# Kernel optimization log

Hardware: AMD Instinct MI355X
Metric: run time of the kernel (lower is better)

The kernel has to match this reference:

```python
import jax, jax.numpy as jnp
import numpy as np
from jax import lax

KSIZE, STRIDE, RATE, FUSE_K, SCALE, FUSE = 3, 1, 2, 3, 10.0, True


def _same_pad(h, w, k, s):
    oh, ow = -(-h // s), -(-w // s)
    ph = max(0, (oh - 1) * s + k - h)
    pw = max(0, (ow - 1) * s + k - w)
    return (ph // 2, ph - ph // 2), (pw // 2, pw - pw // 2), oh, ow


def extract_patches(x, k, s):
    # x: [B,C,H,W] -> ([B, L, C, k, k], Ho, Wo); matches torch Unfold with 'same' padding
    B, C, H, W = x.shape
    (pt, pb), (pl, pr), Ho, Wo = _same_pad(H, W, k, s)
    xp = jnp.pad(x, ((0, 0), (0, 0), (pt, pb), (pl, pr)))
    rows = []
    for i in range(k):
        cols = [xp[:, :, i:i + s * (Ho - 1) + 1:s, j:j + s * (Wo - 1) + 1:s] for j in range(k)]
        rows.append(jnp.stack(cols, axis=2))  # [B,C,k,Ho,Wo]
    pat = jnp.stack(rows, axis=2)  # [B,C,k,k,Ho,Wo]
    pat = pat.reshape(B, C, k, k, Ho * Wo).transpose(0, 4, 1, 2, 3)
    return pat, Ho, Wo


def setup_inputs() -> dict:
    key = jax.random.key(0)
    kf, kb = jax.random.split(key)
    f = jax.random.normal(kf, (2, 128, 64, 64), dtype=jnp.float32)
    b = jax.random.normal(kb, (2, 128, 64, 64), dtype=jnp.float32)
    mask = jnp.zeros((2, 1, 256, 256), dtype=jnp.float32)
    return {"f": f, "b": b, "mask": mask}


def _forward(f, b, mask):
    B, C, Hr, Wr = f.shape
    kernel = 2 * RATE
    # raw background patches used as deconv kernels: [B, L, C, 4, 4]
    raw_w, _, _ = extract_patches(b, kernel, RATE * STRIDE)
    # nearest 1/rate downsample (torch nearest picks every rate-th pixel)
    fd = f[:, :, ::RATE, ::RATE]
    bd = b[:, :, ::RATE, ::RATE]
    Hf, Wf = fd.shape[2], fd.shape[3]
    Hb, Wb = bd.shape[2], bd.shape[3]
    L = Hb * Wb
    w, _, _ = extract_patches(bd, KSIZE, STRIDE)  # [B, L, C, 3, 3]
    # mask -> validity per background patch (original uses batch 0's mask only)
    md = mask[:, :, ::4 * RATE, ::4 * RATE]
    m, _, _ = extract_patches(md, KSIZE, STRIDE)  # [B, L, 1, 3, 3]
    mm = (jnp.mean(m[0], axis=(1, 2, 3)) == 0.0).astype(f.dtype)  # [L]
    # l2-normalize patch kernels (escape_NaN added per element before sum, as in torch)
    wn = w / jnp.sqrt(jnp.sum(w * w + 1e-4, axis=(2, 3, 4), keepdims=True))
    # correlation conv == batched GEMM over extracted foreground patches
    fp, _, _ = extract_patches(fd, KSIZE, 1)  # [B, P=Hf*Wf, C, 3, 3]
    scores = jnp.einsum('bpckl,bqckl->bqp', fp, wn)  # [B, L, Hf*Wf]
    scores = scores.reshape(B, Hb, Wb, Hf, Wf)

    if FUSE:
        def fuse_diag(y2):  # conv with 3x3 identity kernel, same pad == 3 diagonal shifts
            yp = jnp.pad(y2, ((1, 1), (1, 1)))
            return yp[:-2, :-2] + yp[1:-1, 1:-1] + yp[2:, 2:]

        def fuse_one(s):  # [Hb,Wb,Hf,Wf]
            y = fuse_diag(s.reshape(Hb * Wb, Hf * Wf)).reshape(Hb, Wb, Hf, Wf)
            y = y.transpose(1, 0, 3, 2)
            y = fuse_diag(y.reshape(Wb * Hb, Wf * Hf)).reshape(Wb, Hb, Wf, Hf)
            return y.transpose(1, 0, 3, 2)

        scores = jax.vmap(fuse_one)(scores)

    yi = scores.reshape(B, L, Hf, Wf) * mm[None, :, None, None]
    yi = jax.nn.softmax(yi * SCALE, axis=1) * mm[None, :, None, None]

    # transposed conv with per-batch raw patches as kernels (stride=rate, padding=1), /4
    def deconv_one(attn, wpat):  # attn [L,Hf,Wf], wpat [L,C,4,4]
        rhs = jnp.flip(wpat, axis=(2, 3)).transpose(1, 0, 2, 3)  # [C, L, 4, 4]
        pad = kernel - 1 - 1  # equivalent VALID padding for transposed conv with padding=1
        out = lax.conv_general_dilated(attn[None], rhs, (1, 1),
                                       padding=((pad, pad), (pad, pad)),
                                       lhs_dilation=(RATE, RATE),
                                       dimension_numbers=('NCHW', 'OIHW', 'NCHW'))
        return out[0] / 4.0

    y = jax.vmap(deconv_one)(yi, raw_w)  # [B, C, Hr, Wr]
    return y


def reference(f, b, mask):
    return _forward(f, b, mask)
```

## Files before the change

### kernel.cpp

```cpp
#include <hip/hip_runtime.h>
#include <hip/hip_bf16.h>
#include <math.h>

constexpr int HS = 32;
constexpr int Lq = 1024;
constexpr int CN = 128;

typedef short bf16x8 __attribute__((ext_vector_type(8)));
typedef float f32x4  __attribute__((ext_vector_type(4)));

__device__ inline unsigned short f2bf(float x) {
    union { float f; unsigned int u; } c; c.f = x;
    return (unsigned short)((c.u + 0x7FFF + ((c.u >> 16) & 1)) >> 16);
}
__device__ inline float bf2f(unsigned short h) {
    union { unsigned int u; float f; } c; c.u = ((unsigned int)h) << 16;
    return c.f;
}

__global__ __launch_bounds__(256) void k_prep3(const float* __restrict__ f,
                                               const float* __restrict__ bsrc,
                                               unsigned short* __restrict__ fH, unsigned short* __restrict__ fL,
                                               unsigned short* __restrict__ bH, unsigned short* __restrict__ bL,
                                               float* __restrict__ ssq,
                                               unsigned short* __restrict__ Wm) {
    int tx = threadIdx.x;
    if (blockIdx.x < 512) {
        int u = blockIdx.x * 4 + (tx >> 6);
        int lane = tx & 63;
        int p = u & (Lq - 1), bb = u >> 10;
        int py = p >> 5, px = p & 31;
        long srcbase = (((long)bb * CN) * 64 + 2 * py) * 64 + 2 * px;
        float s = 0.f;
#pragma unroll
        for (int i = 0; i < 2; ++i) {
            int c = lane + i * 64;
            long src = srcbase + (long)c * 4096;
            float fv = f[src], bv = bsrc[src];
            int o = u * CN + c;
            unsigned short fh = f2bf(fv), bh = f2bf(bv);
            fH[o] = fh; fL[o] = f2bf(fv - bf2f(fh));
            bH[o] = bh; bL[o] = f2bf(bv - bf2f(bh));
            s += bv * bv;
        }
        for (int off = 32; off > 0; off >>= 1) s += __shfl_down(s, off, 64);
        if (lane == 0) ssq[u] = s;
    } else {
        int idx = (blockIdx.x - 512) * 256 + tx;
        int q  = idx & (Lq - 1);
        int m  = (idx >> 10) & 2047;
        int bb = idx >> 21;
        int c = m >> 4, u = (m >> 2) & 3, v = m & 3;
        int qy = q >> 5, qx = q & 31;
        int y = 2 * qy + u - 1, x = 2 * qx + v - 1;
        float val = 0.f;
        if ((unsigned)y < 64u && (unsigned)x < 64u)
            val = bsrc[(((long)bb * CN + c) * 64 + y) * 64 + x];
        Wm[idx] = f2bf(val);
    }
}

__global__ __launch_bounds__(256) void k_nm(const float* __restrict__ ssq, const float* __restrict__ mask,
                                            float* __restrict__ norms, float* __restrict__ mmb) {
    int idx = blockIdx.x * 256 + threadIdx.x;
    if (idx < 2048) {
        int q = idx & (Lq - 1);
        int bb = idx >> 10;
        int qy = q >> 5, qx = q & 31;
        float s = 0.1152f;
        for (int dk = -1; dk <= 1; ++dk) {
            int y = qy + dk; if ((unsigned)y >= (unsigned)HS) continue;
            for (int dl = -1; dl <= 1; ++dl) {
                int x = qx + dl; if ((unsigned)x >= (unsigned)HS) continue;
                s += ssq[bb * Lq + y * HS + x];
            }
        }
        norms[idx] = sqrtf(s);
    } else {
        int q = idx - 2048;
        int qy = q >> 5, qx = q & 31;
        float s = 0.f;
        for (int dk = -1; dk <= 1; ++dk) {
            int y = qy + dk; if ((unsigned)y >= (unsigned)HS) continue;
            for (int dl = -1; dl <= 1; ++dl) {
                int x = qx + dl; if ((unsigned)x >= (unsigned)HS) continue;
                s += mask[(8 * y) * 256 + 8 * x];
            }
        }
        mmb[q] = (s == 0.0f) ? 1.0f : 0.0f;
    }
}

__global__ __launch_bounds__(256) void k_gram(const unsigned short* __restrict__ fH,
                                              const unsigned short* __restrict__ fL,
                                              const unsigned short* __restrict__ bH,
                                              const unsigned short* __restrict__ bL,
                                              float* __restrict__ GT) {
    const long bz = blockIdx.z;
    const unsigned short* AH = fH + bz * 131072;
    const unsigned short* AL = fL + bz * 131072;
    const unsigned short* BH = bH + bz * 131072;
    const unsigned short* BL = bL + bz * 131072;
    float* C = GT + (bz << 20);
    int t = threadIdx.x, w = t >> 6, lane = t & 63, quad = lane >> 4, l16 = lane & 15;
    int wm = blockIdx.x * 64 + (w & 1) * 32;
    int wn = blockIdx.y * 64 + (w >> 1) * 32;
    int ko = quad * 8;
    f32x4 acc[2][2] = {};
#pragma unroll
    for (int k0 = 0; k0 < 128; k0 += 32) {
        bf16x8 ah0 = *(const bf16x8*)&AH[(wm + l16) * 128 + ko + k0];
        bf16x8 ah1 = *(const bf16x8*)&AH[(wm + 16 + l16) * 128 + ko + k0];
        bf16x8 al0 = *(const bf16x8*)&AL[(wm + l16) * 128 + ko + k0];
        bf16x8 al1 = *(const bf16x8*)&AL[(wm + 16 + l16) * 128 + ko + k0];
        bf16x8 bh0 = *(const bf16x8*)&BH[(wn + l16) * 128 + ko + k0];
        bf16x8 bh1 = *(const bf16x8*)&BH[(wn + 16 + l16) * 128 + ko + k0];
        bf16x8 bl0 = *(const bf16x8*)&BL[(wn + l16) * 128 + ko + k0];
        bf16x8 bl1 = *(const bf16x8*)&BL[(wn + 16 + l16) * 128 + ko + k0];
        acc[0][0] = __builtin_amdgcn_mfma_f32_16x16x32_bf16(ah0, bh0, acc[0][0], 0, 0, 0);
        acc[0][1] = __builtin_amdgcn_mfma_f32_16x16x32_bf16(ah0, bh1, acc[0][1], 0, 0, 0);
        acc[1][0] = __builtin_amdgcn_mfma_f32_16x16x32_bf16(ah1, bh0, acc[1][0], 0, 0, 0);
        acc[1][1] = __builtin_amdgcn_mfma_f32_16x16x32_bf16(ah1, bh1, acc[1][1], 0, 0, 0);
        acc[0][0] = __builtin_amdgcn_mfma_f32_16x16x32_bf16(ah0, bl0, acc[0][0], 0, 0, 0);
        acc[0][1] = __builtin_amdgcn_mfma_f32_16x16x32_bf16(ah0, bl1, acc[0][1], 0, 0, 0);
        acc[1][0] = __builtin_amdgcn_mfma_f32_16x16x32_bf16(ah1, bl0, acc[1][0], 0, 0, 0);
        acc[1][1] = __builtin_amdgcn_mfma_f32_16x16x32_bf16(ah1, bl1, acc[1][1], 0, 0, 0);
        acc[0][0] = __builtin_amdgcn_mfma_f32_16x16x32_bf16(al0, bh0, acc[0][0], 0, 0, 0);
        acc[0][1] = __builtin_amdgcn_mfma_f32_16x16x32_bf16(al0, bh1, acc[0][1], 0, 0, 0);
        acc[1][0] = __builtin_amdgcn_mfma_f32_16x16x32_bf16(al1, bh0, acc[1][0], 0, 0, 0);
        acc[1][1] = __builtin_amdgcn_mfma_f32_16x16x32_bf16(al1, bh1, acc[1][1], 0, 0, 0);
    }
#pragma unroll
    for (int i = 0; i < 2; ++i)
#pragma unroll
        for (int j = 0; j < 2; ++j) {
            int mrow = wm + i * 16 + quad * 4;
            int ncol = wn + j * 16 + l16;
#pragma unroll
            for (int r = 0; r < 4; ++r)
                C[(long)(mrow + r) * Lq + ncol] = acc[i][j][r];
        }
}

__global__ __launch_bounds__(256) void k_s0T(const float* __restrict__ GT, const float* __restrict__ norms,
                                             float* __restrict__ S0T) {
    int idx = blockIdx.x * 256 + threadIdx.x;
    int q  = idx & (Lq - 1);
    int pp = (idx >> 10) & (Lq - 1);
    int bb = idx >> 20;
    int qy = q >> 5, qx = q & 31, py = pp >> 5, px = pp & 31;
    const float* Gb = GT + ((long)bb << 20);
    float s = 0.f;
#pragma unroll
    for (int dk = -1; dk <= 1; ++dk) {
        if ((unsigned)(qy + dk) >= (unsigned)HS || (unsigned)(py + dk) >= (unsigned)HS) continue;
#pragma unroll
        for (int dl = -1; dl <= 1; ++dl) {
            if ((unsigned)(qx + dl) >= (unsigned)HS || (unsigned)(px + dl) >= (unsigned)HS) continue;
            int sft = dk * HS + dl;
            s += Gb[(long)(pp + sft) * Lq + (q + sft)];
        }
    }
    S0T[idx] = s / norms[bb * Lq + q];
}

__global__ __launch_bounds__(256) void k_fuse12(const float* __restrict__ S0, float* __restrict__ S2) {
    int idx = blockIdx.x * 256 + threadIdx.x;
    int p  = idx & (Lq - 1);
    int q  = (idx >> 10) & (Lq - 1);
    int bb = idx >> 20;
    int hb = q >> 5, wb = q & 31, hf = p >> 5, wf = p & 31;
    int ip = wb * HS + hb, jp = wf * HS + hf;
    const float* S = S0 + (long)bb * Lq * Lq;
    float s = 0.f;
#pragma unroll
    for (int d = -1; d <= 1; ++d) {
        int t = ip + d, r = jp + d;
        if ((unsigned)t < (unsigned)Lq && (unsigned)r < (unsigned)Lq) {
            int q2 = (t & 31) * HS + (t >> 5);
            int p2 = (r & 31) * HS + (r >> 5);
            long base = (long)q2 * Lq + p2;
            float v = S[base];
            if (q2 > 0 && p2 > 0)             v += S[base - (Lq + 1)];
            if (q2 < Lq - 1 && p2 < Lq - 1)   v += S[base + (Lq + 1)];
            s += v;
        }
    }
    S2[idx] = s;
}

__global__ __launch_bounds__(256) void k_softmaxT(const float* __restrict__ S2T, const float* __restrict__ mmb,
                                                  unsigned short* __restrict__ At) {
    int wid = blockIdx.x * 4 + (threadIdx.x >> 6);
    int lane = threadIdx.x & 63;
    int bb = wid >> 10, p = wid & (Lq - 1);
    const float* row = S2T + ((long)bb << 20) + (long)p * Lq;
    unsigned short* orow = At + ((long)bb << 20) + (long)p * Lq;
    float x[16]; float mx = -1e30f;
#pragma unroll
    for (int i = 0; i < 16; ++i) {
        int q = i * 64 + lane;
        x[i] = row[q] * mmb[q] * 10.0f;
        mx = fmaxf(mx, x[i]);
    }
    for (int off = 32; off > 0; off >>= 1) mx = fmaxf(mx, __shfl_xor(mx, off, 64));
    float e[16]; float s = 0.f;
#pragma unroll
    for (int i = 0; i < 16; ++i) { e[i] = __expf(x[i] - mx); s += e[i]; }
    for (int off = 32; off > 0; off >>= 1) s += __shfl_xor(s, off, 64);
    float inv = 1.0f / s;
#pragma unroll
    for (int i = 0; i < 16; ++i) {
        int q = i * 64 + lane;
        orow[q] = f2bf(e[i] * mmb[q] * inv);
    }
}

__global__ __launch_bounds__(256) void k_gemm_mfma(const unsigned short* __restrict__ WmA,
                                                   const unsigned short* __restrict__ At,
                                                   float* __restrict__ Cm) {
    const long bz = blockIdx.z;
    const unsigned short* A = WmA + bz * (2048L * Lq);
    const unsigned short* B = At  + bz * ((long)Lq * Lq);
    float* C = Cm + bz * (2048L * Lq);
    __shared__ __align__(16) unsigned short Bs[4096];
    int t = threadIdx.x;
    int w = t >> 6, lane = t & 63;
    int quad = lane >> 4, l16 = lane & 15;
    int m0 = blockIdx.x * 64, n0 = blockIdx.y * 64;
    const unsigned short* aS = A + (long)(m0 + w * 16 + l16) * Lq + quad * 8;
    const unsigned short* bS = B + (long)(n0 + w * 16 + l16) * Lq + quad * 8;
    int sidx = w * 512 + quad * 128 + l16 * 8;
    int fidx = quad * 128 + l16 * 8;
    f32x4 acc0 = {0,0,0,0}, acc1 = {0,0,0,0}, acc2 = {0,0,0,0}, acc3 = {0,0,0,0};
    for (int k0 = 0; k0 < Lq; k0 += 64) {
        bf16x8 bv0 = *(const bf16x8*)(bS + k0);
        bf16x8 bv1 = *(const bf16x8*)(bS + k0 + 32);
        bf16x8 af0 = *(const bf16x8*)(aS + k0);
        bf16x8 af1 = *(const bf16x8*)(aS + k0 + 32);
        __syncthreads();
        *(bf16x8*)&Bs[sidx]        = bv0;
        *(bf16x8*)&Bs[2048 + sidx] = bv1;
        __syncthreads();
#pragma unroll
        for (int kc = 0; kc < 2; ++kc) {
            int o = kc * 2048;
            bf16x8 af = kc ? af1 : af0;
            bf16x8 b0 = *(const bf16x8*)&Bs[o + fidx];
            bf16x8 b1 = *(const bf16x8*)&Bs[o + 512 + fidx];
            bf16x8 b2 = *(const bf16x8*)&Bs[o + 1024 + fidx];
            bf16x8 b3 = *(const bf16x8*)&Bs[o + 1536 + fidx];
            acc0 = __builtin_amdgcn_mfma_f32_16x16x32_bf16(af, b0, acc0, 0, 0, 0);
            acc1 = __builtin_amdgcn_mfma_f32_16x16x32_bf16(af, b1, acc1, 0, 0, 0);
            acc2 = __builtin_amdgcn_mfma_f32_16x16x32_bf16(af, b2, acc2, 0, 0, 0);
            acc3 = __builtin_amdgcn_mfma_f32_16x16x32_bf16(af, b3, acc3, 0, 0, 0);
        }
    }
    int mrow = m0 + w * 16 + quad * 4;
#pragma unroll
    for (int r = 0; r < 4; ++r) {
        C[(long)(mrow + r) * Lq + n0 +  0 + l16] = acc0[r];
        C[(long)(mrow + r) * Lq + n0 + 16 + l16] = acc1[r];
        C[(long)(mrow + r) * Lq + n0 + 32 + l16] = acc2[r];
        C[(long)(mrow + r) * Lq + n0 + 48 + l16] = acc3[r];
    }
}

__global__ __launch_bounds__(256) void k_epi2(const float* __restrict__ P, float* __restrict__ out) {
    int idx = blockIdx.x * 256 + threadIdx.x;
    int ox = idx & 63, oy = (idx >> 6) & 63, c = (idx >> 12) & 127, bb = idx >> 19;
    const float* Pb = P + (long)bb * 2048 * Lq;
    float s = 0.f;
#pragma unroll
    for (int u = 0; u < 4; ++u) {
        int t = oy + u - 2;
        if (t & 1) continue;
        int iy = t >> 1;
        if ((unsigned)iy >= (unsigned)HS) continue;
#pragma unroll
        for (int v = 0; v < 4; ++v) {
            int r = ox + v - 2;
            if (r & 1) continue;
            int ix = r >> 1;
            if ((unsigned)ix >= (unsigned)HS) continue;
            s += Pb[(long)((c << 4) + (3 - u) * 4 + (3 - v)) * Lq + (iy << 5) + ix];
        }
    }
    out[idx] = 0.25f * s;
}

extern "C" void kernel_launch(void* const* d_in, const int* in_sizes, int n_in,
                              void* d_out, int out_size, void* d_ws, size_t ws_size,
                              hipStream_t stream) {
    const float* f    = (const float*)d_in[0];
    const float* bsrc = (const float*)d_in[1];
    const float* mask = (const float*)d_in[2];
    float* out = (float*)d_out;
    float* ws = (float*)d_ws;

    float* ssq   = ws;
    float* norms = ssq   + 2048;
    float* mmb   = norms + 2048;
    unsigned short* fH = (unsigned short*)(mmb + 1024);
    unsigned short* fL = fH + 262144;
    unsigned short* bH = fL + 262144;
    unsigned short* bL = bH + 262144;
    float* GTa   = (float*)(bL + 262144);
    float* C1    = GTa + 2097152;
    float* C2    = C1  + 2097152;
    unsigned short* Wm = (unsigned short*)(C2 + 2097152);
    float* S0T  = C1;
    float* S2T  = C2;
    unsigned short* attnT = (unsigned short*)GTa;
    float* P    = C1;

    hipLaunchKernelGGL(k_prep3,     dim3(16896),      dim3(256), 0, stream, f, bsrc, fH, fL, bH, bL, ssq, Wm);
    hipLaunchKernelGGL(k_nm,        dim3(12),         dim3(256), 0, stream, ssq, mask, norms, mmb);
    hipLaunchKernelGGL(k_gram,      dim3(16, 16, 2),  dim3(256), 0, stream, fH, fL, bH, bL, GTa);
    hipLaunchKernelGGL(k_s0T,       dim3(8192),       dim3(256), 0, stream, GTa, norms, S0T);
    hipLaunchKernelGGL(k_fuse12,    dim3(8192),       dim3(256), 0, stream, S0T, S2T);
    hipLaunchKernelGGL(k_softmaxT,  dim3(512),        dim3(256), 0, stream, S2T, mmb, attnT);
    hipLaunchKernelGGL(k_gemm_mfma, dim3(32, 16, 2),  dim3(256), 0, stream, Wm, attnT, P);
    hipLaunchKernelGGL(k_epi2,      dim3(4096),       dim3(256), 0, stream, P, out);
}
```

Baseline: 155.4 us.

## Retile deconv GEMM to 128x64 blocks with direct global-to-LDS loads

The deconv GEMM block tile grows from 64x64 to 128x64, arranged as a 2x2 warp grid where each warp holds 4x2 MFMA accumulators. Both A and B tiles are now staged through LDS using global_load_lds instead of register round-trips. The aim is more reuse per LDS read and fewer VGPR-mediated copies, which should cut global traffic and instruction overhead. The grid halves in size, and the LDS row stride of 64 bf16 with no padding may cause bank conflicts on the fragment reads.

```diff
diff --git a/kernel.cpp b/kernel.cpp
--- a/kernel.cpp
+++ b/kernel.cpp
@@ -16,6 +16,12 @@
 __device__ inline float bf2f(unsigned short h) {
     union { unsigned int u; float f; } c; c.u = ((unsigned int)h) << 16;
     return c.f;
+}
+
+__device__ inline void gload16(const void* g, void* l) {
+    __builtin_amdgcn_global_load_lds(
+        (const __attribute__((address_space(1))) unsigned int*)g,
+        (__attribute__((address_space(3))) unsigned int*)l, 16, 0, 0);
 }
 
 __global__ __launch_bounds__(256) void k_prep3(const float* __restrict__ f,
@@ -223,46 +229,52 @@
     const unsigned short* A = WmA + bz * (2048L * Lq);
     const unsigned short* B = At  + bz * ((long)Lq * Lq);
     float* C = Cm + bz * (2048L * Lq);
-    __shared__ __align__(16) unsigned short Bs[4096];
+    __shared__ __align__(16) unsigned short As[128 * 64];
+    __shared__ __align__(16) unsigned short Bs[64 * 64];
     int t = threadIdx.x;
-    int w = t >> 6, lane = t & 63;
-    int quad = lane >> 4, l16 = lane & 15;
-    int m0 = blockIdx.x * 64, n0 = blockIdx.y * 64;
-    const unsigned short* aS = A + (long)(m0 + w * 16 + l16) * Lq + quad * 8;
-    const unsigned short* bS = B + (long)(n0 + w * 16 + l16) * Lq + quad * 8;
-    int sidx = w * 512 + quad * 128 + l16 * 8;
-    int fidx = quad * 128 + l16 * 8;
-    f32x4 acc0 = {0,0,0,0}, acc1 = {0,0,0,0}, acc2 = {0,0,0,0}, acc3 = {0,0,0,0};
+    int w = t >> 6, lane = t & 63, quad = lane >> 4, l16 = lane & 15;
+    int wr = w >> 1, wc = w & 1;
+    int m0 = blockIdx.x * 128, n0 = blockIdx.y * 64;
+    int srow = t >> 3;
+    int scol = (t & 7) * 8;
+    f32x4 acc[4][2] = {};
     for (int k0 = 0; k0 < Lq; k0 += 64) {
-        bf16x8 bv0 = *(const bf16x8*)(bS + k0);
-        bf16x8 bv1 = *(const bf16x8*)(bS + k0 + 32);
-        bf16x8 af0 = *(const bf16x8*)(aS + k0);
-        bf16x8 af1 = *(const bf16x8*)(aS + k0 + 32);
         __syncthreads();
-        *(bf16x8*)&Bs[sidx]        = bv0;
-        *(bf16x8*)&Bs[2048 + sidx] = bv1;
+#pragma unroll
+        for (int r = 0; r < 4; ++r)
+            gload16(A + (long)(m0 + r * 32 + srow) * Lq + k0 + scol,
+                    &As[(r * 32 + srow) * 64 + scol]);
+#pragma unroll
+        for (int r = 0; r < 2; ++r)
+            gload16(B + (long)(n0 + r * 32 + srow) * Lq + k0 + scol,
+                    &Bs[(r * 32 + srow) * 64 + scol]);
         __syncthreads();
 #pragma unroll
-        for (int kc = 0; kc < 2; ++kc) {
-            int o = kc * 2048;
-            bf16x8 af = kc ? af1 : af0;
-            bf16x8 b0 = *(const bf16x8*)&Bs[o + fidx];
-            bf16x8 b1 = *(const bf16x8*)&Bs[o + 512 + fidx];
-            bf16x8 b2 = *(const bf16x8*)&Bs[o + 1024 + fidx];
-            bf16x8 b3 = *(const bf16x8*)&Bs[o + 1536 + fidx];
-            acc0 = __builtin_amdgcn_mfma_f32_16x16x32_bf16(af, b0, acc0, 0, 0, 0);
-            acc1 = __builtin_amdgcn_mfma_f32_16x16x32_bf16(af, b1, acc1, 0, 0, 0);
-            acc2 = __builtin_amdgcn_mfma_f32_16x16x32_bf16(af, b2, acc2, 0, 0, 0);
-            acc3 = __builtin_amdgcn_mfma_f32_16x16x32_bf16(af, b3, acc3, 0, 0, 0);
-        }
-    }
-    int mrow = m0 + w * 16 + quad * 4;
-#pragma unroll
-    for (int r = 0; r < 4; ++r) {
-        C[(long)(mrow + r) * Lq + n0 +  0 + l16] = acc0[r];
-        C[(long)(mrow + r) * Lq + n0 + 16 + l16] = acc1[r];
-        C[(long)(mrow + r) * Lq + n0 + 32 + l16] = acc2[r];
-        C[(long)(mrow + r) * Lq + n0 + 48 + l16] = acc3[r];
+        for (int ks = 0; ks < 2; ++ks) {
+            bf16x8 a[4], b[2];
+#pragma unroll
+            for (int i = 0; i < 4; ++i)
+                a[i] = *(const bf16x8*)&As[(wr * 64 + i * 16 + l16) * 64 + ks * 32 + quad * 8];
+#pragma unroll
+            for (int j = 0; j < 2; ++j)
+                b[j] = *(const bf16x8*)&Bs[(wc * 32 + j * 16 + l16) * 64 + ks * 32 + quad * 8];
+#pragma unroll
+            for (int i = 0; i < 4; ++i)
+#pragma unroll
+                for (int j = 0; j < 2; ++j)
+                    acc[i][j] = __builtin_amdgcn_mfma_f32_16x16x32_bf16(a[i], b[j], acc[i][j], 0, 0, 0);
+        }
+    }
+#pragma unroll
+    for (int i = 0; i < 4; ++i) {
+        int mrow = m0 + wr * 64 + i * 16 + quad * 4;
+#pragma unroll
+        for (int j = 0; j < 2; ++j) {
+            int ncol = n0 + wc * 32 + j * 16 + l16;
+#pragma unroll
+            for (int r = 0; r < 4; ++r)
+                C[(long)(mrow + r) * Lq + ncol] = acc[i][j][r];
+        }
     }
 }
 
@@ -320,6 +332,6 @@
     hipLaunchKernelGGL(k_s0T,       dim3(8192),       dim3(256), 0, stream, GTa, norms, S0T);
     hipLaunchKernelGGL(k_fuse12,    dim3(8192),       dim3(256), 0, stream, S0T, S2T);
     hipLaunchKernelGGL(k_softmaxT,  dim3(512),        dim3(256), 0, stream, S2T, mmb, attnT);
-    hipLaunchKernelGGL(k_gemm_mfma, dim3(32, 16, 2),  dim3(256), 0, stream, Wm, attnT, P);
+    hipLaunchKernelGGL(k_gemm_mfma, dim3(16, 16, 2),  dim3(256), 0, stream, Wm, attnT, P);
     hipLaunchKernelGGL(k_epi2,      dim3(4096),       dim3(256), 0, stream, P, out);
 }
```

New measurement: 144.0 us. 7.3% less time.
